# Kernel optimization log

Hardware: AMD Instinct MI355X
Metric: run time of the kernel (lower is better)

The kernel has to match this reference:

```python
import jax, jax.numpy as jnp
import numpy as np

N_NODES = 50000
IN_CH = 128
OUT_CH = 64
HID = 2 * OUT_CH  # 128
N_EDGES = 800000


def sage_conv(x, src, dst, W_l, b_l, W_r):
    """PyG SAGEConv with mean aggregation:
       out = mean_{j in N(i)} x_j @ W_l + b_l + x_i @ W_r
    """
    n = x.shape[0]
    msg = x[src]  # [E, D] gather
    agg = jax.ops.segment_sum(msg, dst, num_segments=n)
    cnt = jax.ops.segment_sum(jnp.ones((src.shape[0],), x.dtype), dst, num_segments=n)
    mean = agg / jnp.maximum(cnt, 1.0)[:, None]
    return mean @ W_l + b_l + x @ W_r


def setup_inputs() -> dict:
    key = jax.random.key(0)
    ks = jax.random.split(key, 12)
    x = jax.random.normal(ks[0], (N_NODES, IN_CH), dtype=jnp.float32)
    edge_index = jax.random.randint(ks[1], (2, N_EDGES), 0, N_NODES, dtype=jnp.int64)

    def glorot(k, shape):
        fan_in, fan_out = shape
        lim = jnp.sqrt(6.0 / (fan_in + fan_out)).astype(jnp.float32)
        return jax.random.uniform(k, shape, jnp.float32, -lim, lim)

    return {
        "x": x,
        "edge_index": edge_index,
        "W1_l": glorot(ks[2], (IN_CH, HID)),
        "b1": jnp.zeros((HID,), jnp.float32),
        "W1_r": glorot(ks[3], (IN_CH, HID)),
        "Wmu_l": glorot(ks[4], (HID, OUT_CH)),
        "bmu": jnp.zeros((OUT_CH,), jnp.float32),
        "Wmu_r": glorot(ks[5], (HID, OUT_CH)),
        "Wls_l": glorot(ks[6], (HID, OUT_CH)),
        "bls": jnp.zeros((OUT_CH,), jnp.float32),
        "Wls_r": glorot(ks[7], (HID, OUT_CH)),
    }


def reference(x, edge_index, W1_l, b1, W1_r, Wmu_l, bmu, Wmu_r, Wls_l, bls, Wls_r):
    src, dst = edge_index[0], edge_index[1]
    h = jax.nn.relu(sage_conv(x, src, dst, W1_l, b1, W1_r))  # [N, HID]
    mu = sage_conv(h, src, dst, Wmu_l, bmu, Wmu_r)            # [N, OUT]
    logstd = sage_conv(h, src, dst, Wls_l, bls, Wls_r)        # [N, OUT]
    return (mu, logstd)
```

## Files before the change

kernel.cpp:

```cpp
#include <hip/hip_runtime.h>

#define NODES_CH 128
#define OUTW 64


__global__ void k_zero(int* __restrict__ p, int n) {
    int i = blockIdx.x * blockDim.x + threadIdx.x;
    if (i < n) p[i] = 0;
}

__global__ void k_degree(const int* __restrict__ dstI, int* __restrict__ deg, int E) {
    int e = blockIdx.x * blockDim.x + threadIdx.x;
    if (e < E) atomicAdd(&deg[dstI[e]], 1);
}

__global__ __launch_bounds__(1024)
void k_scan(const int* __restrict__ deg, int* __restrict__ rp,
            int* __restrict__ cursor, int n) {
    __shared__ int wsum[16];
    int tid  = threadIdx.x;
    int lane = tid & 63;
    int wid  = tid >> 6;
    int carry = 0;
    for (int base = 0; base < n; base += 1024) {
        int i = base + tid;
        int v = (i < n) ? deg[i] : 0;
        int x = v;
        #pragma unroll
        for (int off = 1; off < 64; off <<= 1) {
            int t = __shfl_up(x, off, 64);
            if (lane >= off) x += t;
        }
        if (lane == 63) wsum[wid] = x;
        __syncthreads();
        if (wid == 0) {
            int y = (lane < 16) ? wsum[lane] : 0;
            #pragma unroll
            for (int off = 1; off < 16; off <<= 1) {
                int t = __shfl_up(y, off, 64);
                if (lane >= off) y += t;
            }
            if (lane < 16) wsum[lane] = y;
        }
        __syncthreads();
        int woff  = (wid > 0) ? wsum[wid - 1] : 0;
        int incl  = x + woff;
        int total = wsum[15];
        if (i < n) {
            int ex = carry + incl - v;
            rp[i] = ex;
            cursor[i] = ex;
        }
        carry += total;
        __syncthreads();
    }
    if (tid == 0) rp[n] = carry;
}

__global__ void k_fill(const int* __restrict__ srcI, const int* __restrict__ dstI,
                       int* __restrict__ cursor, int* __restrict__ colA, int E) {
    int e = blockIdx.x * blockDim.x + threadIdx.x;
    if (e < E) {
        int d = dstI[e];
        int p = atomicAdd(&cursor[d], 1);
        colA[p] = srcI[e];
    }
}

__global__ __launch_bounds__(256)
void k_agg(const float* __restrict__ X, const int* __restrict__ rp,
           const int* __restrict__ colA, float* __restrict__ out, int n) {
    int node = (blockIdx.x << 2) + (threadIdx.x >> 6);
    if (node >= n) return;
    int lane = threadIdx.x & 63;
    int eh = lane >> 5;
    int c4 = lane & 31;
    int beg = rp[node], end = rp[node + 1];
    const float4* __restrict__ X4 = (const float4*)X;
    float4 s = make_float4(0.f, 0.f, 0.f, 0.f);
    int e = beg + eh;
    for (; e + 2 < end; e += 4) {
        int c0 = colA[e];
        int c1 = colA[e + 2];
        float4 v0 = X4[(size_t)c0 * 32 + c4];
        float4 v1 = X4[(size_t)c1 * 32 + c4];
        s.x += v0.x + v1.x; s.y += v0.y + v1.y;
        s.z += v0.z + v1.z; s.w += v0.w + v1.w;
    }
    if (e < end) {
        int c0 = colA[e];
        float4 v0 = X4[(size_t)c0 * 32 + c4];
        s.x += v0.x; s.y += v0.y; s.z += v0.z; s.w += v0.w;
    }
    s.x += __shfl_xor(s.x, 32);
    s.y += __shfl_xor(s.y, 32);
    s.z += __shfl_xor(s.z, 32);
    s.w += __shfl_xor(s.w, 32);
    if (eh == 0) {
        float inv = 1.f / (float)((end > beg) ? (end - beg) : 1);
        ((float4*)out)[(size_t)node * 32 + c4] =
            make_float4(s.x * inv, s.y * inv, s.z * inv, s.w * inv);
    }
}

template <int MODE>
__global__ __launch_bounds__(256, 2)
void k_gemm(const float* __restrict__ A0, const float* __restrict__ A1,
            const float* __restrict__ Wa0, const float* __restrict__ Wb0,
            const float* __restrict__ Wa1, const float* __restrict__ Wb1,
            const float* __restrict__ ba, const float* __restrict__ bb,
            float* __restrict__ out0, float* __restrict__ out1, int N) {
    __shared__ float Wlds[64 * 128];
    const int tid = threadIdx.x;
    const int cg  = tid & 15;
    const int rg  = tid >> 4;
    const int rbase = blockIdx.x * 64 + rg * 4;

    float acc[4][8];
    #pragma unroll
    for (int r = 0; r < 4; r++)
        #pragma unroll
        for (int c = 0; c < 8; c++) acc[r][c] = 0.f;

    for (int phase = 0; phase < 2; ++phase) {
        const float* __restrict__ A = phase ? A1 : A0;
        for (int kc = 0; kc < 2; ++kc) {
            __syncthreads();
            if (MODE == 0) {
                const float* __restrict__ W = phase ? Wa1 : Wa0;
                for (int i = tid; i < 2048; i += 256) {
                    int kr = i >> 5, c4 = i & 31;
                    ((float4*)Wlds)[i] =
                        *(const float4*)(W + (size_t)(kc * 64 + kr) * 128 + c4 * 4);
                }
            } else {
                const float* __restrict__ WA = phase ? Wa1 : Wa0;
                const float* __restrict__ WB = phase ? Wb1 : Wb0;
                for (int i = tid; i < 2048; i += 256) {
                    int kr = i >> 5, c4 = i & 31;
                    const float* s = (c4 < 16)
                        ? (WA + (size_t)(kc * 64 + kr) * 64 + c4 * 4)
                        : (WB + (size_t)(kc * 64 + kr) * 64 + (c4 - 16) * 4);
                    ((float4*)Wlds)[i] = *(const float4*)s;
                }
            }
            __syncthreads();
            #pragma unroll 2
            for (int k = 0; k < 64; k += 4) {
                float4 a[4];
                #pragma unroll
                for (int r = 0; r < 4; r++) {
                    int row = rbase + r;
                    a[r] = (row < N)
                        ? *(const float4*)(A + (size_t)row * 128 + kc * 64 + k)
                        : make_float4(0.f, 0.f, 0.f, 0.f);
                }
                #pragma unroll
                for (int kk = 0; kk < 4; kk++) {
                    float4 w0 = *(const float4*)(Wlds + (k + kk) * 128 + cg * 4);
                    float4 w1 = *(const float4*)(Wlds + (k + kk) * 128 + 64 + cg * 4);
                    #pragma unroll
                    for (int r = 0; r < 4; r++) {
                        float av = (kk == 0) ? a[r].x : (kk == 1) ? a[r].y
                                 : (kk == 2) ? a[r].z : a[r].w;
                        acc[r][0] += av * w0.x;
                        acc[r][1] += av * w0.y;
                        acc[r][2] += av * w0.z;
                        acc[r][3] += av * w0.w;
                        acc[r][4] += av * w1.x;
                        acc[r][5] += av * w1.y;
                        acc[r][6] += av * w1.z;
                        acc[r][7] += av * w1.w;
                    }
                }
            }
        }
    }

    if (MODE == 0) {
        const float4 bv0 = *(const float4*)(ba + cg * 4);
        const float4 bv1 = *(const float4*)(ba + 64 + cg * 4);
        #pragma unroll
        for (int r = 0; r < 4; r++) {
            int row = rbase + r;
            if (row >= N) continue;
            float4 v0, v1;
            v0.x = fmaxf(acc[r][0] + bv0.x, 0.f);
            v0.y = fmaxf(acc[r][1] + bv0.y, 0.f);
            v0.z = fmaxf(acc[r][2] + bv0.z, 0.f);
            v0.w = fmaxf(acc[r][3] + bv0.w, 0.f);
            v1.x = fmaxf(acc[r][4] + bv1.x, 0.f);
            v1.y = fmaxf(acc[r][5] + bv1.y, 0.f);
            v1.z = fmaxf(acc[r][6] + bv1.z, 0.f);
            v1.w = fmaxf(acc[r][7] + bv1.w, 0.f);
            *(float4*)(out0 + (size_t)row * 128 + cg * 4) = v0;
            *(float4*)(out0 + (size_t)row * 128 + 64 + cg * 4) = v1;
        }
    } else {
        const float4 bm = *(const float4*)(ba + cg * 4);
        const float4 bl = *(const float4*)(bb + cg * 4);
        #pragma unroll
        for (int r = 0; r < 4; r++) {
            int row = rbase + r;
            if (row >= N) continue;
            float4 vm, vl;
            vm.x = acc[r][0] + bm.x; vm.y = acc[r][1] + bm.y;
            vm.z = acc[r][2] + bm.z; vm.w = acc[r][3] + bm.w;
            vl.x = acc[r][4] + bl.x; vl.y = acc[r][5] + bl.y;
            vl.z = acc[r][6] + bl.z; vl.w = acc[r][7] + bl.w;
            *(float4*)(out0 + (size_t)row * 64 + cg * 4) = vm;
            *(float4*)(out1 + (size_t)row * 64 + cg * 4) = vl;
        }
    }
}


extern "C" void kernel_launch(void* const* d_in, const int* in_sizes, int n_in,
                              void* d_out, int out_size, void* d_ws, size_t ws_size,
                              hipStream_t stream) {
    const float* x     = (const float*)d_in[0];
    const int*   ei    = (const int*)d_in[1];
    const float* W1_l  = (const float*)d_in[2];
    const float* b1    = (const float*)d_in[3];
    const float* W1_r  = (const float*)d_in[4];
    const float* Wmu_l = (const float*)d_in[5];
    const float* bmu   = (const float*)d_in[6];
    const float* Wmu_r = (const float*)d_in[7];
    const float* Wls_l = (const float*)d_in[8];
    const float* bls   = (const float*)d_in[9];
    const float* Wls_r = (const float*)d_in[10];

    const int N = in_sizes[0] / NODES_CH;
    const int E = in_sizes[1] / 2;
    const int* srcI = ei;
    const int* dstI = ei + E;

    const int NP = (N + 63) & ~63;
    const int EP = (E + 15) & ~15;

    char* w = (char*)d_ws;
    int* deg    = (int*)w;  w += (size_t)NP * 4;
    int* rp     = (int*)w;  w += (size_t)(NP + 64) * 4;
    int* cursor = (int*)w;  w += (size_t)NP * 4;
    int* colA   = (int*)w;  w += (size_t)EP * 4;
    float* meanb = (float*)w;  w += (size_t)N * 128 * 4;
    float* h     = (float*)w;  w += (size_t)N * 128 * 4;

    float* out_mu = (float*)d_out;
    float* out_ls = out_mu + (size_t)N * OUTW;

    k_zero<<<(N + 255) / 256, 256, 0, stream>>>(deg, N);
    k_degree<<<(E + 255) / 256, 256, 0, stream>>>(dstI, deg, E);
    k_scan<<<1, 1024, 0, stream>>>(deg, rp, cursor, N);
    k_fill<<<(E + 255) / 256, 256, 0, stream>>>(srcI, dstI, cursor, colA, E);

    const int ablocks = (N + 3) / 4;
    const int gblocks = (N + 63) / 64;

    k_agg<<<ablocks, 256, 0, stream>>>(x, rp, colA, meanb, N);
    k_gemm<0><<<gblocks, 256, 0, stream>>>(
        meanb, x, W1_l, nullptr, W1_r, nullptr, b1, nullptr, h, nullptr, N);

    k_agg<<<ablocks, 256, 0, stream>>>(h, rp, colA, meanb, N);
    k_gemm<1><<<gblocks, 256, 0, stream>>>(
        meanb, h, Wmu_l, Wls_l, Wmu_r, Wls_r, bmu, bls, out_mu, out_ls, N);
}
```

Before: 539.7 us.

## Aggregate from channel-segmented feature layout and shrink GEMM row tile

Repacks node features into 8 channel segments of 16 floats each, so every aggregation pass gathers a 6.4MB slice that can stay cache-resident, using a 2D grid over nodes and segments. The first GEMM also writes h in this segmented layout, so the second aggregation needs no extra repack. The GEMM tile shrinks from 64 to 32 rows with 32-wide K chunks, giving more blocks and less shared memory. In exchange it adds a repack kernel, an extra N×128 buffer and an extra write of h, and falls back to the old path if the workspace is too small.

New measurement: 643.6 us. 1.19x slower.

```diff
diff --git a/kernel.cpp b/kernel.cpp
--- a/kernel.cpp
+++ b/kernel.cpp
@@ -67,9 +67,45 @@
     }
 }
 
+__global__ void k_repack(const float* __restrict__ X, float* __restrict__ XS, int n) {
+    int i = blockIdx.x * blockDim.x + threadIdx.x;
+    if (i >= n * 32) return;
+    int node = i >> 5, c4 = i & 31;
+    float4 v = ((const float4*)X)[i];
+    ((float4*)XS)[(size_t)(c4 >> 2) * n * 4 + (size_t)node * 4 + (c4 & 3)] = v;
+}
+
 __global__ __launch_bounds__(256)
-void k_agg(const float* __restrict__ X, const int* __restrict__ rp,
-           const int* __restrict__ colA, float* __restrict__ out, int n) {
+void k_agg_seg(const float* __restrict__ XS, const int* __restrict__ rp,
+               const int* __restrict__ colA, float* __restrict__ out, int n) {
+    int node = (blockIdx.x << 2) + (threadIdx.x >> 6);
+    if (node >= n) return;
+    int lane = threadIdx.x & 63;
+    int es = lane >> 3;
+    int ch = lane & 7;
+    int seg = blockIdx.y;
+    int beg = rp[node], end = rp[node + 1];
+    const float2* __restrict__ XS2 = (const float2*)XS;
+    size_t segbase = (size_t)seg * n * 8;
+    float2 s = make_float2(0.f, 0.f);
+    for (int e = beg + es; e < end; e += 8) {
+        int c = colA[e];
+        float2 v = XS2[segbase + (size_t)c * 8 + ch];
+        s.x += v.x; s.y += v.y;
+    }
+    s.x += __shfl_xor(s.x, 8);  s.y += __shfl_xor(s.y, 8);
+    s.x += __shfl_xor(s.x, 16); s.y += __shfl_xor(s.y, 16);
+    s.x += __shfl_xor(s.x, 32); s.y += __shfl_xor(s.y, 32);
+    if (es == 0) {
+        float inv = 1.f / (float)((end > beg) ? (end - beg) : 1);
+        ((float2*)out)[(size_t)node * 64 + seg * 8 + ch] =
+            make_float2(s.x * inv, s.y * inv);
+    }
+}
+
+__global__ __launch_bounds__(256)
+void k_agg_row(const float* __restrict__ X, const int* __restrict__ rp,
+               const int* __restrict__ colA, float* __restrict__ out, int n) {
     int node = (blockIdx.x << 2) + (threadIdx.x >> 6);
     if (node >= n) return;
     int lane = threadIdx.x & 63;
@@ -103,56 +139,57 @@
     }
 }
 
-template <int MODE>
+template <int MODE, int SEGOUT>
 __global__ __launch_bounds__(256, 2)
 void k_gemm(const float* __restrict__ A0, const float* __restrict__ A1,
             const float* __restrict__ Wa0, const float* __restrict__ Wb0,
             const float* __restrict__ Wa1, const float* __restrict__ Wb1,
             const float* __restrict__ ba, const float* __restrict__ bb,
-            float* __restrict__ out0, float* __restrict__ out1, int N) {
-    __shared__ float Wlds[64 * 128];
+            float* __restrict__ out0, float* __restrict__ out1,
+            float* __restrict__ outseg, int N) {
+    __shared__ float Wlds[32 * 128];
     const int tid = threadIdx.x;
     const int cg  = tid & 15;
     const int rg  = tid >> 4;
-    const int rbase = blockIdx.x * 64 + rg * 4;
-
-    float acc[4][8];
+    const int rbase = blockIdx.x * 32 + rg * 2;
+
+    float acc[2][8];
     #pragma unroll
-    for (int r = 0; r < 4; r++)
+    for (int r = 0; r < 2; r++)
         #pragma unroll
         for (int c = 0; c < 8; c++) acc[r][c] = 0.f;
 
     for (int phase = 0; phase < 2; ++phase) {
         const float* __restrict__ A = phase ? A1 : A0;
-        for (int kc = 0; kc < 2; ++kc) {
+        for (int kc = 0; kc < 4; ++kc) {
             __syncthreads();
             if (MODE == 0) {
                 const float* __restrict__ W = phase ? Wa1 : Wa0;
-                for (int i = tid; i < 2048; i += 256) {
+                for (int i = tid; i < 1024; i += 256) {
                     int kr = i >> 5, c4 = i & 31;
                     ((float4*)Wlds)[i] =
-                        *(const float4*)(W + (size_t)(kc * 64 + kr) * 128 + c4 * 4);
+                        *(const float4*)(W + (size_t)(kc * 32 + kr) * 128 + c4 * 4);
                 }
             } else {
                 const float* __restrict__ WA = phase ? Wa1 : Wa0;
                 const float* __restrict__ WB = phase ? Wb1 : Wb0;
-                for (int i = tid; i < 2048; i += 256) {
+                for (int i = tid; i < 1024; i += 256) {
                     int kr = i >> 5, c4 = i & 31;
                     const float* s = (c4 < 16)
-                        ? (WA + (size_t)(kc * 64 + kr) * 64 + c4 * 4)
-                        : (WB + (size_t)(kc * 64 + kr) * 64 + (c4 - 16) * 4);
+                        ? (WA + (size_t)(kc * 32 + kr) * 64 + c4 * 4)
+                        : (WB + (size_t)(kc * 32 + kr) * 64 + (c4 - 16) * 4);
                     ((float4*)Wlds)[i] = *(const float4*)s;
                 }
             }
             __syncthreads();
             #pragma unroll 2
-            for (int k = 0; k < 64; k += 4) {
-                float4 a[4];
+            for (int k = 0; k < 32; k += 4) {
+                float4 a[2];
                 #pragma unroll
-                for (int r = 0; r < 4; r++) {
+                for (int r = 0; r < 2; r++) {
                     int row = rbase + r;
                     a[r] = (row < N)
-                        ? *(const float4*)(A + (size_t)row * 128 + kc * 64 + k)
+                        ? *(const float4*)(A + (size_t)row * 128 + kc * 32 + k)
                         : make_float4(0.f, 0.f, 0.f, 0.f);
                 }
                 #pragma unroll
@@ -160,7 +197,7 @@
                     float4 w0 = *(const float4*)(Wlds + (k + kk) * 128 + cg * 4);
                     float4 w1 = *(const float4*)(Wlds + (k + kk) * 128 + 64 + cg * 4);
                     #pragma unroll
-                    for (int r = 0; r < 4; r++) {
+                    for (int r = 0; r < 2; r++) {
                         float av = (kk == 0) ? a[r].x : (kk == 1) ? a[r].y
                                  : (kk == 2) ? a[r].z : a[r].w;
                         acc[r][0] += av * w0.x;
@@ -181,7 +218,7 @@
         const float4 bv0 = *(const float4*)(ba + cg * 4);
         const float4 bv1 = *(const float4*)(ba + 64 + cg * 4);
         #pragma unroll
-        for (int r = 0; r < 4; r++) {
+        for (int r = 0; r < 2; r++) {
             int row = rbase + r;
             if (row >= N) continue;
             float4 v0, v1;
@@ -195,12 +232,18 @@
             v1.w = fmaxf(acc[r][7] + bv1.w, 0.f);
             *(float4*)(out0 + (size_t)row * 128 + cg * 4) = v0;
             *(float4*)(out0 + (size_t)row * 128 + 64 + cg * 4) = v1;
+            if (SEGOUT) {
+                *(float4*)(outseg + (size_t)(cg >> 2) * N * 16
+                           + (size_t)row * 16 + (cg & 3) * 4) = v0;
+                *(float4*)(outseg + (size_t)(4 + (cg >> 2)) * N * 16
+                           + (size_t)row * 16 + (cg & 3) * 4) = v1;
+            }
         }
     } else {
         const float4 bm = *(const float4*)(ba + cg * 4);
         const float4 bl = *(const float4*)(bb + cg * 4);
         #pragma unroll
-        for (int r = 0; r < 4; r++) {
+        for (int r = 0; r < 2; r++) {
             int row = rbase + r;
             if (row >= N) continue;
             float4 vm, vl;
@@ -245,6 +288,10 @@
     int* colA   = (int*)w;  w += (size_t)EP * 4;
     float* meanb = (float*)w;  w += (size_t)N * 128 * 4;
     float* h     = (float*)w;  w += (size_t)N * 128 * 4;
+    float* segb  = (float*)w;  w += (size_t)N * 128 * 4;
+
+    const bool use_seg =
+        ((size_t)((char*)(segb + (size_t)N * 128) - (char*)d_ws)) <= ws_size;
 
     float* out_mu = (float*)d_out;
     float* out_ls = out_mu + (size_t)N * OUTW;
@@ -255,13 +302,27 @@
     k_fill<<<(E + 255) / 256, 256, 0, stream>>>(srcI, dstI, cursor, colA, E);
 
     const int ablocks = (N + 3) / 4;
-    const int gblocks = (N + 63) / 64;
-
-    k_agg<<<ablocks, 256, 0, stream>>>(x, rp, colA, meanb, N);
-    k_gemm<0><<<gblocks, 256, 0, stream>>>(
-        meanb, x, W1_l, nullptr, W1_r, nullptr, b1, nullptr, h, nullptr, N);
-
-    k_agg<<<ablocks, 256, 0, stream>>>(h, rp, colA, meanb, N);
-    k_gemm<1><<<gblocks, 256, 0, stream>>>(
-        meanb, h, Wmu_l, Wls_l, Wmu_r, Wls_r, bmu, bls, out_mu, out_ls, N);
-}
+    const int gblocks = (N + 31) / 32;
+
+    if (use_seg) {
+        const dim3 agrid(ablocks, 8);
+        k_repack<<<(N * 32 + 255) / 256, 256, 0, stream>>>(x, segb, N);
+        k_agg_seg<<<agrid, 256, 0, stream>>>(segb, rp, colA, meanb, N);
+        k_gemm<0, 1><<<gblocks, 256, 0, stream>>>(
+            meanb, x, W1_l, nullptr, W1_r, nullptr, b1, nullptr,
+            h, nullptr, segb, N);
+        k_agg_seg<<<agrid, 256, 0, stream>>>(segb, rp, colA, meanb, N);
+        k_gemm<1, 0><<<gblocks, 256, 0, stream>>>(
+            meanb, h, Wmu_l, Wls_l, Wmu_r, Wls_r, bmu, bls,
+            out_mu, out_ls, nullptr, N);
+    } else {
+        k_agg_row<<<ablocks, 256, 0, stream>>>(x, rp, colA, meanb, N);
+        k_gemm<0, 0><<<gblocks, 256, 0, stream>>>(
+            meanb, x, W1_l, nullptr, W1_r, nullptr, b1, nullptr,
+            h, nullptr, nullptr, N);
+        k_agg_row<<<ablocks, 256, 0, stream>>>(h, rp, colA, meanb, N);
+        k_gemm<1, 0><<<gblocks, 256, 0, stream>>>(
+            meanb, h, Wmu_l, Wls_l, Wmu_r, Wls_r, bmu, bls,
+            out_mu, out_ls, nullptr, N);
+    }
+}
```
